# Performance work log

Measured on AMD Instinct MI355X. Metric: run time of the kernel, lower is better.

Reference implementation:

```python
import jax, jax.numpy as jnp
import numpy as np

E = 8   # number of experts (= laac_size)
A = 8   # number of agents
B = 2048
S = 256   # per-agent input feature size
H1, H2 = 512, 256          # shallow_dims
D0, D1, D2 = 256, 512, 128  # deep_dims


def setup_inputs() -> dict:
    key = jax.random.key(0)
    ks = jax.random.split(key, 11)
    inputs = jax.random.normal(ks[0], (A, B, S), dtype=jnp.float32)
    laac_shallow = jax.random.randint(ks[1], (1, A), 0, E, dtype=jnp.int64)
    laac_deep = jax.random.randint(ks[2], (1, A), 0, E, dtype=jnp.int64)
    def w(k, shape, fan_in):
        return jax.random.normal(k, shape, dtype=jnp.float32) / np.sqrt(fan_in)
    return {
        "inputs": inputs,
        "laac_shallow": laac_shallow,
        "laac_deep": laac_deep,
        "Ws1": w(ks[3], (E, S, H1), S),  "bs1": jnp.zeros((E, H1), jnp.float32),
        "Ws2": w(ks[4], (E, H1, H2), H1), "bs2": jnp.zeros((E, H2), jnp.float32),
        "Wd1": w(ks[5], (E, D0, D1), D0), "bd1": jnp.zeros((E, D1), jnp.float32),
        "Wd2": w(ks[6], (E, D1, D2), D1), "bd2": jnp.zeros((E, D2), jnp.float32),
    }


def reference(inputs, laac_shallow, laac_deep, Ws1, bs1, Ws2, bs2, Wd1, bd1, Wd2, bd2):
    agent_ids = jnp.arange(A)
    # --- shallow experts: every expert applied to full stacked input [A,B,S] ---
    # Linear -> ReLU -> Linear -> ReLU (final_activation)
    h = jax.nn.relu(jnp.einsum('abi,eih->eabh', inputs, Ws1) + bs1[:, None, None, :])  # [E,A,B,H1]
    sh = jax.nn.relu(jnp.einsum('eabh,eho->eabo', h, Ws2) + bs2[:, None, None, :])     # [E,A,B,H2]
    sel_s = laac_shallow.T[:, 0]             # [A] expert id per agent
    deep_in = sh[sel_s, agent_ids]           # gather over expert dim -> [A,B,H2]
    # --- deep experts: Linear -> ReLU -> Linear (no final activation) ---
    d = jax.nn.relu(jnp.einsum('abi,eih->eabh', deep_in, Wd1) + bd1[:, None, None, :])  # [E,A,B,D1]
    dout = jnp.einsum('eabh,eho->eabo', d, Wd2) + bd2[:, None, None, :]                 # [E,A,B,D2]
    sel_d = laac_deep.T[:, 0]
    out = dout[sel_d, agent_ids]             # [A,B,D2] (original returns this split per agent)
    return out
```

## Files before the change

### kernel.cpp

```cpp
#include <hip/hip_runtime.h>
#include <hip/hip_bf16.h>


typedef __attribute__((ext_vector_type(8))) short bf16x8;
typedef __attribute__((ext_vector_type(4))) float f32x4;

__device__ __forceinline__ ushort f2b(float x) {
    __hip_bfloat16 h = __float2bfloat16(x);
    return *reinterpret_cast<ushort*>(&h);
}

__global__ __launch_bounds__(256)
void prep_weights(const float* __restrict__ Ws1, const float* __restrict__ Ws2,
                  const float* __restrict__ Wd1, const float* __restrict__ Wd2,
                  ushort* __restrict__ W1p, ushort* __restrict__ W2p,
                  ushort* __restrict__ W3p, ushort* __restrict__ W4p)
{
    const int layer = blockIdx.z;
    const int e  = blockIdx.y;
    const int fg = blockIdx.x;
    const float* W; ushort* Wp; int K, N;
    if (layer == 0)      { W = Ws1; Wp = W1p; K = 256; N = 512; }
    else if (layer == 1) { W = Ws2; Wp = W2p; K = 512; N = 256; }
    else if (layer == 2) { W = Wd1; Wp = W3p; K = 256; N = 512; }
    else                 { W = Wd2; Wp = W4p; K = 512; N = 128; }
    if (fg >= N / 16) return;
    const int NK = K / 32;
    W += (size_t)e * K * N;

    __shared__ float tile[512][17];
    const int tid = threadIdx.x;
    const int n0 = fg * 16;
    for (int idx = tid; idx < K * 16; idx += 256)
        tile[idx >> 4][idx & 15] = W[(size_t)(idx >> 4) * N + n0 + (idx & 15)];
    __syncthreads();
    ushort* dst = Wp + (((size_t)e * (N / 16) + fg) * NK) * 512;
    for (int w = tid; w < NK * 64; w += 256) {
        const int s    = w >> 6;
        const int lane = w & 63;
        const int c    = lane & 15;
        const int kb   = s * 32 + ((lane >> 4) << 3);
        bf16x8 v;
        #pragma unroll
        for (int j = 0; j < 8; ++j)
            v[j] = (short)f2b(tile[kb + j][c]);
        *reinterpret_cast<bf16x8*>(&dst[(size_t)w * 8]) = v;
    }
}

template<int K, int N, int MG, int RELU>
__device__ __forceinline__ void layer_mlp(
    const ushort* __restrict__ Wp, const float* __restrict__ bias,
    const ushort* __restrict__ sIn, ushort* __restrict__ sOut,
    float* __restrict__ gOut, int wid, int lane)
{
    constexpr int NG = 16 / MG;
    constexpr int F  = N / 16 / NG;
    constexpr int M4 = 4 / MG;
    constexpr int NK = K / 32;
    const int r15 = lane & 15, lh = lane >> 4;
    const int wc = wid % NG, wr = wid / NG;
    const int rowBase = wr * (64 / MG);

    const ushort* bBase = Wp + ((size_t)(wc * F) * NK) * 512 + (size_t)lane * 8;

    f32x4 acc[M4][F];
    #pragma unroll
    for (int m = 0; m < M4; ++m)
        #pragma unroll
        for (int f = 0; f < F; ++f)
            acc[m][f] = (f32x4){0.f, 0.f, 0.f, 0.f};

    #pragma unroll
    for (int s = 0; s < NK; ++s) {
        const int k0 = s * 32;
        bf16x8 a[M4];
        #pragma unroll
        for (int m = 0; m < M4; ++m) {
            const int row  = rowBase + m * 16 + r15;
            const int phys = ((k0 >> 3) + lh) ^ (row & 7);
            a[m] = *reinterpret_cast<const bf16x8*>(
                reinterpret_cast<const char*>(sIn) + row * (K * 2) + (phys << 4));
        }
        bf16x8 b[F];
        #pragma unroll
        for (int f = 0; f < F; ++f)
            b[f] = *reinterpret_cast<const bf16x8*>(
                bBase + ((size_t)f * NK + s) * 512);
        #pragma unroll
        for (int m = 0; m < M4; ++m)
            #pragma unroll
            for (int f = 0; f < F; ++f)
                acc[m][f] = __builtin_amdgcn_mfma_f32_16x16x32_bf16(
                    b[f], a[m], acc[m][f], 0, 0, 0);
    }

    #pragma unroll
    for (int f = 0; f < F; ++f) {
        const int cbase = (wc * F + f) * 16 + lh * 4;
        const float4 bv = *reinterpret_cast<const float4*>(&bias[cbase]);
        #pragma unroll
        for (int m = 0; m < M4; ++m) {
            const int row = rowBase + m * 16 + r15;
            float v0 = acc[m][f][0] + bv.x;
            float v1 = acc[m][f][1] + bv.y;
            float v2 = acc[m][f][2] + bv.z;
            float v3 = acc[m][f][3] + bv.w;
            if (RELU) {
                v0 = fmaxf(v0, 0.f); v1 = fmaxf(v1, 0.f);
                v2 = fmaxf(v2, 0.f); v3 = fmaxf(v3, 0.f);
            }
            if (gOut) {
                *reinterpret_cast<float4*>(&gOut[(size_t)row * N + cbase]) =
                    (float4){v0, v1, v2, v3};
            } else {
                const uint lo = ((uint)f2b(v1) << 16) | (uint)f2b(v0);
                const uint hi = ((uint)f2b(v3) << 16) | (uint)f2b(v2);
                const int byteoff = row * (N * 2) +
                    ((((cbase >> 3) ^ (row & 7))) << 4) + ((cbase & 7) << 1);
                *reinterpret_cast<uint2*>(
                    reinterpret_cast<char*>(sOut) + byteoff) = (uint2){lo, hi};
            }
        }
    }
}

__global__ __launch_bounds__(1024, 4)
void madps_fused(const float* __restrict__ X,
                 const int* __restrict__ sel_s, const int* __restrict__ sel_d,
                 const ushort* __restrict__ W1p, const ushort* __restrict__ W2p,
                 const ushort* __restrict__ W3p, const ushort* __restrict__ W4p,
                 const float* __restrict__ bs1, const float* __restrict__ bs2,
                 const float* __restrict__ bd1, const float* __restrict__ bd2,
                 float* __restrict__ out)
{
    constexpr int S = 256, H1 = 512, H2 = 256, D1 = 512, D2 = 128;

    __shared__ __align__(16) ushort buf0[64 * 256];
    __shared__ __align__(16) ushort buf1[64 * 512];

    const int bid   = blockIdx.x;
    const int agent = bid & 7;
    const int rb    = bid >> 3;
    const int tid   = threadIdx.x;
    const int lane  = tid & 63;
    const int wid   = tid >> 6;

    const long long es = sel_s[agent];
    const long long ed = sel_d[agent];

    const float* Xa = X + ((size_t)agent * 2048 + (size_t)rb * 64) * S;

    #pragma unroll
    for (int i = 0; i < 4; ++i) {
        const int flat4 = i * 1024 + tid;
        const int row = flat4 >> 6;
        const int c4  = flat4 & 63;
        const float4 v = reinterpret_cast<const float4*>(Xa)[flat4];
        ushort4 o;
        o.x = f2b(v.x); o.y = f2b(v.y); o.z = f2b(v.z); o.w = f2b(v.w);
        const int byteoff = (((c4 >> 1) ^ (row & 7)) << 4) | ((c4 & 1) << 3);
        *reinterpret_cast<ushort4*>(
            reinterpret_cast<char*>(buf0) + row * 512 + byteoff) = o;
    }
    __syncthreads();

    layer_mlp<S, H1, 1, 1>(W1p + (size_t)es * ((H1 / 16) * (S / 32) * 512),
                           bs1 + es * H1, buf0, buf1, nullptr, wid, lane);
    __syncthreads();
    layer_mlp<H1, H2, 1, 1>(W2p + (size_t)es * ((H2 / 16) * (H1 / 32) * 512),
                            bs2 + es * H2, buf1, buf0, nullptr, wid, lane);
    __syncthreads();
    layer_mlp<H2, D1, 1, 1>(W3p + (size_t)ed * ((D1 / 16) * (H2 / 32) * 512),
                            bd1 + ed * D1, buf0, buf1, nullptr, wid, lane);
    __syncthreads();
    float* outP = out + ((size_t)agent * 2048 + (size_t)rb * 64) * D2;
    layer_mlp<D1, D2, 2, 0>(W4p + (size_t)ed * ((D2 / 16) * (D1 / 32) * 512),
                            bd2 + ed * D2, buf1, nullptr, outP, wid, lane);
}

extern "C" void kernel_launch(void* const* d_in, const int* in_sizes, int n_in,
                              void* d_out, int out_size, void* d_ws, size_t ws_size,
                              hipStream_t stream)
{
    constexpr int E = 8, S = 256, H1 = 512, H2 = 256, D1 = 512, D2 = 128;

    const float* inputs = (const float*)d_in[0];
    const int*   sel_s  = (const int*)d_in[1];
    const int*   sel_d  = (const int*)d_in[2];
    const float* Ws1 = (const float*)d_in[3];
    const float* bs1 = (const float*)d_in[4];
    const float* Ws2 = (const float*)d_in[5];
    const float* bs2 = (const float*)d_in[6];
    const float* Wd1 = (const float*)d_in[7];
    const float* bd1 = (const float*)d_in[8];
    const float* Wd2 = (const float*)d_in[9];
    const float* bd2 = (const float*)d_in[10];
    float* out = (float*)d_out;

    ushort* W1p = (ushort*)d_ws;
    ushort* W2p = W1p + (size_t)E * S * H1;
    ushort* W3p = W2p + (size_t)E * H1 * H2;
    ushort* W4p = W3p + (size_t)E * H2 * D1;

    prep_weights<<<dim3(32, E, 4), 256, 0, stream>>>(
        Ws1, Ws2, Wd1, Wd2, W1p, W2p, W3p, W4p);

    madps_fused<<<dim3(256), dim3(1024), 0, stream>>>(
        inputs, sel_s, sel_d, W1p, W2p, W3p, W4p,
        bs1, bs2, bd1, bd2, out);
}
```

Baseline: 34.15 us.

## Switch first three MLP layers to 32x32x16 MFMA with new weight packing

Layers one to three now use the 32x32x16 bf16 MFMA instead of 16x16x32. A new prep kernel packs the weights into 32-column fragments, and the LDS swizzle gains a row-dependent term (sig) to avoid bank conflicts. When a wave holds only one accumulator, two accumulators alternate across k steps to break the MFMA dependency chain. The aim is fewer MFMA issues and less B-fragment loading per FLOP. In exchange, accumulators need more registers, and weight prep now takes an extra kernel launch.

```diff
diff --git a/kernel.cpp b/kernel.cpp
--- a/kernel.cpp
+++ b/kernel.cpp
@@ -4,63 +4,163 @@
 
 typedef __attribute__((ext_vector_type(8))) short bf16x8;
 typedef __attribute__((ext_vector_type(4))) float f32x4;
+typedef __attribute__((ext_vector_type(16))) float f32x16;
 
 __device__ __forceinline__ ushort f2b(float x) {
     __hip_bfloat16 h = __float2bfloat16(x);
     return *reinterpret_cast<ushort*>(&h);
 }
+__device__ __forceinline__ int sig(int row) { return (row + (row >> 3)) & 7; }
 
 __global__ __launch_bounds__(256)
-void prep_weights(const float* __restrict__ Ws1, const float* __restrict__ Ws2,
-                  const float* __restrict__ Wd1, const float* __restrict__ Wd2,
-                  ushort* __restrict__ W1p, ushort* __restrict__ W2p,
-                  ushort* __restrict__ W3p, ushort* __restrict__ W4p)
-{
-    const int layer = blockIdx.z;
-    const int e  = blockIdx.y;
-    const int fg = blockIdx.x;
+void prep32(const float* __restrict__ Ws1, const float* __restrict__ Ws2,
+            const float* __restrict__ Wd1,
+            ushort* __restrict__ W1p, ushort* __restrict__ W2p,
+            ushort* __restrict__ W3p)
+{
+    const int layer = blockIdx.z, e = blockIdx.y, cg = blockIdx.x;
     const float* W; ushort* Wp; int K, N;
     if (layer == 0)      { W = Ws1; Wp = W1p; K = 256; N = 512; }
     else if (layer == 1) { W = Ws2; Wp = W2p; K = 512; N = 256; }
-    else if (layer == 2) { W = Wd1; Wp = W3p; K = 256; N = 512; }
-    else                 { W = Wd2; Wp = W4p; K = 512; N = 128; }
-    if (fg >= N / 16) return;
-    const int NK = K / 32;
+    else                 { W = Wd1; Wp = W3p; K = 256; N = 512; }
+    if (cg >= N / 32) return;
+    const int NK = K / 16;
     W += (size_t)e * K * N;
 
+    __shared__ float tile[512][33];
+    const int tid = threadIdx.x;
+    for (int idx = tid; idx < K * 32; idx += 256)
+        tile[idx >> 5][idx & 31] = W[(size_t)(idx >> 5) * N + cg * 32 + (idx & 31)];
+    __syncthreads();
+    ushort* dst = Wp + (((size_t)e * (N / 32) + cg) * NK) * 512;
+    for (int w = tid; w < NK * 64; w += 256) {
+        const int s = w >> 6, lane = w & 63;
+        const int c  = lane & 31;
+        const int kb = s * 16 + ((lane >> 5) << 3);
+        bf16x8 v;
+        #pragma unroll
+        for (int j = 0; j < 8; ++j) v[j] = (short)f2b(tile[kb + j][c]);
+        *reinterpret_cast<bf16x8*>(&dst[(size_t)w * 8]) = v;
+    }
+}
+
+__global__ __launch_bounds__(256)
+void prep16(const float* __restrict__ Wd2, ushort* __restrict__ W4p)
+{
+    const int e = blockIdx.y, fg = blockIdx.x;
+    constexpr int K = 512, N = 128, NK = K / 32;
+    const float* W = Wd2 + (size_t)e * K * N;
     __shared__ float tile[512][17];
     const int tid = threadIdx.x;
     const int n0 = fg * 16;
     for (int idx = tid; idx < K * 16; idx += 256)
         tile[idx >> 4][idx & 15] = W[(size_t)(idx >> 4) * N + n0 + (idx & 15)];
     __syncthreads();
-    ushort* dst = Wp + (((size_t)e * (N / 16) + fg) * NK) * 512;
+    ushort* dst = W4p + (((size_t)e * (N / 16) + fg) * NK) * 512;
     for (int w = tid; w < NK * 64; w += 256) {
-        const int s    = w >> 6;
-        const int lane = w & 63;
-        const int c    = lane & 15;
-        const int kb   = s * 32 + ((lane >> 4) << 3);
+        const int s = w >> 6, lane = w & 63;
+        const int c  = lane & 15;
+        const int kb = s * 32 + ((lane >> 4) << 3);
         bf16x8 v;
         #pragma unroll
-        for (int j = 0; j < 8; ++j)
-            v[j] = (short)f2b(tile[kb + j][c]);
+        for (int j = 0; j < 8; ++j) v[j] = (short)f2b(tile[kb + j][c]);
         *reinterpret_cast<bf16x8*>(&dst[(size_t)w * 8]) = v;
     }
 }
 
 template<int K, int N, int MG, int RELU>
-__device__ __forceinline__ void layer_mlp(
+__device__ __forceinline__ void layer32(
     const ushort* __restrict__ Wp, const float* __restrict__ bias,
     const ushort* __restrict__ sIn, ushort* __restrict__ sOut,
-    float* __restrict__ gOut, int wid, int lane)
+    int wid, int lane)
 {
     constexpr int NG = 16 / MG;
-    constexpr int F  = N / 16 / NG;
-    constexpr int M4 = 4 / MG;
-    constexpr int NK = K / 32;
+    constexpr int F  = N / 32 / NG;
+    constexpr int M4 = 2 / MG;
+    constexpr int NK = K / 16;
+    constexpr int SP = (M4 * F == 1) ? 2 : 1;
+    const int l31 = lane & 31, hi = lane >> 5;
+    const int wc = wid % NG, wr = wid / NG;
+    const int rowBase = (MG == 1) ? 0 : wr * 32;
+
+    const ushort* bBase = Wp + ((size_t)(wc * F) * NK) * 512 + (size_t)lane * 8;
+
+    f32x16 acc[M4][F][SP];
+    #pragma unroll
+    for (int m = 0; m < M4; ++m)
+        #pragma unroll
+        for (int f = 0; f < F; ++f)
+            #pragma unroll
+            for (int p = 0; p < SP; ++p)
+                #pragma unroll
+                for (int t = 0; t < 16; ++t)
+                    acc[m][f][p][t] = 0.f;
+
+    #pragma unroll
+    for (int s = 0; s < NK; ++s) {
+        bf16x8 a[M4];
+        #pragma unroll
+        for (int m = 0; m < M4; ++m) {
+            const int row  = rowBase + m * 32 + l31;
+            const int phys = (2 * s + hi) ^ sig(row);
+            a[m] = *reinterpret_cast<const bf16x8*>(
+                reinterpret_cast<const char*>(sIn) + row * (K * 2) + (phys << 4));
+        }
+        bf16x8 b[F];
+        #pragma unroll
+        for (int f = 0; f < F; ++f)
+            b[f] = *reinterpret_cast<const bf16x8*>(
+                bBase + ((size_t)f * NK + s) * 512);
+        #pragma unroll
+        for (int m = 0; m < M4; ++m)
+            #pragma unroll
+            for (int f = 0; f < F; ++f) {
+                const int p = (SP == 2) ? (s & 1) : 0;
+                acc[m][f][p] = __builtin_amdgcn_mfma_f32_32x32x16_bf16(
+                    b[f], a[m], acc[m][f][p], 0, 0, 0);
+            }
+    }
+
+    #pragma unroll
+    for (int m = 0; m < M4; ++m) {
+        const int row = rowBase + m * 32 + l31;
+        #pragma unroll
+        for (int f = 0; f < F; ++f) {
+            #pragma unroll
+            for (int q = 0; q < 4; ++q) {
+                const int cbase = (wc * F + f) * 32 + 8 * q + 4 * hi;
+                const float4 bq = *reinterpret_cast<const float4*>(&bias[cbase]);
+                const float bArr[4] = {bq.x, bq.y, bq.z, bq.w};
+                float v[4];
+                #pragma unroll
+                for (int t = 0; t < 4; ++t) {
+                    float x = acc[m][f][0][4 * q + t];
+                    if (SP == 2) x += acc[m][f][1][4 * q + t];
+                    x += bArr[t];
+                    if (RELU) x = fmaxf(x, 0.f);
+                    v[t] = x;
+                }
+                const uint lo = ((uint)f2b(v[1]) << 16) | (uint)f2b(v[0]);
+                const uint hh = ((uint)f2b(v[3]) << 16) | (uint)f2b(v[2]);
+                const int byteoff = row * (N * 2) +
+                    (((cbase >> 3) ^ sig(row)) << 4) + ((cbase & 7) << 1);
+                *reinterpret_cast<uint2*>(
+                    reinterpret_cast<char*>(sOut) + byteoff) = (uint2){lo, hh};
+            }
+        }
+    }
+}
+
+template<int K, int N, int RELU>
+__device__ __forceinline__ void layer16(
+    const ushort* __restrict__ Wp, const float* __restrict__ bias,
+    const ushort* __restrict__ sIn, float* __restrict__ gOut,
+    int wid, int lane)
+{
+    constexpr int NG = 8, F = N / 16 / NG, M4 = 2, NK = K / 32;
     const int r15 = lane & 15, lh = lane >> 4;
     const int wc = wid % NG, wr = wid / NG;
-    const int rowBase = wr * (64 / MG);
+    const int rowBase = wr * 32;
 
     const ushort* bBase = Wp + ((size_t)(wc * F) * NK) * 512 + (size_t)lane * 8;
 
@@ -73,12 +173,11 @@
 
     #pragma unroll
     for (int s = 0; s < NK; ++s) {
-        const int k0 = s * 32;
         bf16x8 a[M4];
         #pragma unroll
         for (int m = 0; m < M4; ++m) {
             const int row  = rowBase + m * 16 + r15;
-            const int phys = ((k0 >> 3) + lh) ^ (row & 7);
+            const int phys = (4 * s + lh) ^ sig(row);
             a[m] = *reinterpret_cast<const bf16x8*>(
                 reinterpret_cast<const char*>(sIn) + row * (K * 2) + (phys << 4));
         }
@@ -98,29 +197,20 @@
     #pragma unroll
     for (int f = 0; f < F; ++f) {
         const int cbase = (wc * F + f) * 16 + lh * 4;
-        const float4 bv = *reinterpret_cast<const float4*>(&bias[cbase]);
+        const float4 bq = *reinterpret_cast<const float4*>(&bias[cbase]);
         #pragma unroll
         for (int m = 0; m < M4; ++m) {
             const int row = rowBase + m * 16 + r15;
-            float v0 = acc[m][f][0] + bv.x;
-            float v1 = acc[m][f][1] + bv.y;
-            float v2 = acc[m][f][2] + bv.z;
-            float v3 = acc[m][f][3] + bv.w;
+            float v0 = acc[m][f][0] + bq.x;
+            float v1 = acc[m][f][1] + bq.y;
+            float v2 = acc[m][f][2] + bq.z;
+            float v3 = acc[m][f][3] + bq.w;
             if (RELU) {
                 v0 = fmaxf(v0, 0.f); v1 = fmaxf(v1, 0.f);
                 v2 = fmaxf(v2, 0.f); v3 = fmaxf(v3, 0.f);
             }
-            if (gOut) {
-                *reinterpret_cast<float4*>(&gOut[(size_t)row * N + cbase]) =
-                    (float4){v0, v1, v2, v3};
-            } else {
-                const uint lo = ((uint)f2b(v1) << 16) | (uint)f2b(v0);
-                const uint hi = ((uint)f2b(v3) << 16) | (uint)f2b(v2);
-                const int byteoff = row * (N * 2) +
-                    ((((cbase >> 3) ^ (row & 7))) << 4) + ((cbase & 7) << 1);
-                *reinterpret_cast<uint2*>(
-                    reinterpret_cast<char*>(sOut) + byteoff) = (uint2){lo, hi};
-            }
+            *reinterpret_cast<float4*>(&gOut[(size_t)row * N + cbase]) =
+                (float4){v0, v1, v2, v3};
         }
     }
 }
@@ -159,24 +249,24 @@
         const float4 v = reinterpret_cast<const float4*>(Xa)[flat4];
         ushort4 o;
         o.x = f2b(v.x); o.y = f2b(v.y); o.z = f2b(v.z); o.w = f2b(v.w);
-        const int byteoff = (((c4 >> 1) ^ (row & 7)) << 4) | ((c4 & 1) << 3);
+        const int byteoff = (((c4 >> 1) ^ sig(row)) << 4) | ((c4 & 1) << 3);
         *reinterpret_cast<ushort4*>(
             reinterpret_cast<char*>(buf0) + row * 512 + byteoff) = o;
     }
     __syncthreads();
 
-    layer_mlp<S, H1, 1, 1>(W1p + (size_t)es * ((H1 / 16) * (S / 32) * 512),
-                           bs1 + es * H1, buf0, buf1, nullptr, wid, lane);
-    __syncthreads();
-    layer_mlp<H1, H2, 1, 1>(W2p + (size_t)es * ((H2 / 16) * (H1 / 32) * 512),
-                            bs2 + es * H2, buf1, buf0, nullptr, wid, lane);
-    __syncthreads();
-    layer_mlp<H2, D1, 1, 1>(W3p + (size_t)ed * ((D1 / 16) * (H2 / 32) * 512),
-                            bd1 + ed * D1, buf0, buf1, nullptr, wid, lane);
+    layer32<S, H1, 1, 1>(W1p + (size_t)es * (S * H1), bs1 + es * H1,
+                         buf0, buf1, wid, lane);
+    __syncthreads();
+    layer32<H1, H2, 2, 1>(W2p + (size_t)es * (H1 * H2), bs2 + es * H2,
+                          buf1, buf0, wid, lane);
+    __syncthreads();
+    layer32<H2, D1, 1, 1>(W3p + (size_t)ed * (H2 * D1), bd1 + ed * D1,
+                          buf0, buf1, wid, lane);
     __syncthreads();
     float* outP = out + ((size_t)agent * 2048 + (size_t)rb * 64) * D2;
-    layer_mlp<D1, D2, 2, 0>(W4p + (size_t)ed * ((D2 / 16) * (D1 / 32) * 512),
-                            bd2 + ed * D2, buf1, nullptr, outP, wid, lane);
+    layer16<D1, D2, 0>(W4p + (size_t)ed * (D1 * D2), bd2 + ed * D2,
+                       buf1, outP, wid, lane);
 }
 
 extern "C" void kernel_launch(void* const* d_in, const int* in_sizes, int n_in,
@@ -203,8 +293,8 @@
     ushort* W3p = W2p + (size_t)E * H1 * H2;
     ushort* W4p = W3p + (size_t)E * H2 * D1;
 
-    prep_weights<<<dim3(32, E, 4), 256, 0, stream>>>(
-        Ws1, Ws2, Wd1, Wd2, W1p, W2p, W3p, W4p);
+    prep32<<<dim3(16, E, 3), 256, 0, stream>>>(Ws1, Ws2, Wd1, W1p, W2p, W3p);
+    prep16<<<dim3(8, E, 1), 256, 0, stream>>>(Wd2, W4p);
 
     madps_fused<<<dim3(256), dim3(1024), 0, stream>>>(
         inputs, sel_s, sel_d, W1p, W2p, W3p, W4p,
```

Result: slower. 39.64 us (+16.1%).
